# Optimization experiments

Hardware: AMD Instinct MI355X
Metric: run time of the kernel (lower is better)

The kernel has to match this reference:

```python
import jax, jax.numpy as jnp
import numpy as np

WS = 7          # window size
NH = 12         # num heads
DIM = 384       # channels
B, H, W = 16, 56, 56
N = WS * WS     # 49 tokens per window
HD = DIM // NH  # head dim = 32
SCALE = HD ** (-0.5)


def _rel_pos_index():
    # matches the numpy construction in Window_MSA.__init__
    coords = np.stack(np.meshgrid(np.arange(WS), np.arange(WS), indexing='ij'))
    flat = coords.reshape(2, -1)                      # [2, 49]
    rel = flat[:, :, None] - flat[:, None, :]         # [2, 49, 49]
    rel = rel.transpose(1, 2, 0)                      # [49, 49, 2]
    rel[:, :, 0] += WS - 1
    rel[:, :, 1] += WS - 1
    rel[:, :, 0] *= 2 * WS - 1
    return rel.sum(-1)                                # [49, 49] int

_REL_IDX = jnp.asarray(_rel_pos_index())


def setup_inputs() -> dict:
    key = jax.random.key(0)
    ks = jax.random.split(key, 4)
    return {
        'x': jax.random.normal(ks[0], (B, H, W, DIM), dtype=jnp.float32),
        'qkv_w': jax.random.normal(ks[1], (DIM, 3 * DIM), dtype=jnp.float32) * 0.02,
        'qkv_b': jnp.zeros((3 * DIM,), dtype=jnp.float32),
        'proj_w': jax.random.normal(ks[2], (DIM, DIM), dtype=jnp.float32) * 0.02,
        'proj_b': jnp.zeros((DIM,), dtype=jnp.float32),
        'rel_table': jax.random.normal(ks[3], ((2 * WS - 1) ** 2, NH), dtype=jnp.float32) * 0.02,
    }


def reference(x, qkv_w, qkv_b, proj_w, proj_b, rel_table):
    b, h, w, c = x.shape
    nwh, nww = h // WS, w // WS
    # window partition -> [B*nW, N, C]
    xw = x.reshape(b, nwh, WS, nww, WS, c).transpose(0, 1, 3, 2, 4, 5)
    xw = xw.reshape(-1, N, c)
    bn = xw.shape[0]
    # qkv projection -> q,k,v each [bn, NH, N, HD]
    qkv = (xw @ qkv_w + qkv_b).reshape(bn, N, 3, NH, HD).transpose(2, 0, 3, 1, 4)
    q, k, v = qkv[0] * SCALE, qkv[1], qkv[2]
    attn = jax.nn.softmax(jnp.einsum('bhnd,bhmd->bhnm', q, k), axis=-1)
    # NOTE: source adds relative position bias AFTER softmax (faithful quirk)
    bias = rel_table[_REL_IDX.reshape(-1)].reshape(N, N, NH).transpose(2, 0, 1)
    attn = attn + bias[None]
    out = jnp.einsum('bhnm,bhmd->bhnd', attn, v)
    out = out.transpose(0, 2, 1, 3).reshape(bn, N, c)
    out = out @ proj_w + proj_b
    # window reverse -> [B, H, W, C]
    out = out.reshape(b, nwh, nww, WS, WS, c).transpose(0, 1, 3, 2, 4, 5)
    return out.reshape(b, h, w, c)
```

## Files before the change

### kernel.cpp

```cpp
#include <hip/hip_runtime.h>
#include <hip/hip_bf16.h>

typedef unsigned short u16;
typedef __attribute__((ext_vector_type(8))) short bf16x8;
typedef __attribute__((ext_vector_type(4))) float f32x4;

#define NH 12
#define SCALE 0.1767766952966369f

#define UNIT 20992
#define WS_R0    ((size_t)0)
#define WS_QKVB  ((size_t)12288 * UNIT)
#define WS_PROJB (WS_QKVB + (size_t)3 * 12 * 49152)
#define WS_NEED  (WS_PROJB + (size_t)12 * 49152)

__device__ __forceinline__ void split2(float x, u16& h, u16& l) {
    __hip_bfloat16 hb = __float2bfloat16(x);
    float hf = __bfloat162float(hb);
    __hip_bfloat16 lb = __float2bfloat16(x - hf);
    h = __bfloat16_as_ushort(hb);
    l = __bfloat16_as_ushort(lb);
}
__device__ __forceinline__ void split8(const float* v, bf16x8& hi, bf16x8& lo) {
    #pragma unroll
    for (int j = 0; j < 8; ++j) {
        u16 h, l; split2(v[j], h, l);
        hi[j] = (short)h; lo[j] = (short)l;
    }
}

__device__ __forceinline__ void gload16(const char* g, char* l) {
    __builtin_amdgcn_global_load_lds(
        (const __attribute__((address_space(1))) unsigned*)g,
        (__attribute__((address_space(3))) unsigned*)l, 16, 0, 0);
}

__device__ __forceinline__ int swz(int row, int g) {
    return row * 128 + (((g ^ (row & 7)) & 7) << 4);
}

__global__ __launch_bounds__(384) void prep_kernel(
    const float* __restrict__ qkv_w, const float* __restrict__ proj_w,
    char* __restrict__ ws)
{
    const int b = blockIdx.x, row = threadIdx.x;
    float w; size_t base;
    int kl;
    if (b < 1152) {
        int s = b / 384, r = b % 384, ck = r / 32; kl = r % 32;
        w = qkv_w[(size_t)(ck * 32 + kl) * 1152 + s * 384 + row];
        base = WS_QKVB + (size_t)(s * 12 + ck) * 49152;
    } else {
        int b1 = b - 1152, ck = b1 / 32; kl = b1 % 32;
        w = proj_w[(size_t)(ck * 32 + kl) * 384 + row];
        base = WS_PROJB + (size_t)ck * 49152;
    }
    u16 h, l; split2(w, h, l);
    int o = ((row >> 4) * 4 + (kl >> 3)) * 256 + (row & 15) * 16 + (kl & 7) * 2;
    *(u16*)(ws + base + o)         = h;
    *(u16*)(ws + base + 24576 + o) = l;
}

__global__ __launch_bounds__(512, 4) void qkv_gemm_kernel(
    const float* __restrict__ x, const char* __restrict__ wsB,
    const float* __restrict__ qkv_b, char* __restrict__ ws)
{
    __shared__ __align__(16) char bt[49152];

    const int bid = blockIdx.x;
    const int nt = bid % 6, s = nt >> 1, lt = nt & 1;
    const int pair = bid / 6;
    const int tid = threadIdx.x, lane = tid & 63;
    const int wv = tid >> 6;
    const int wm = wv >> 1, wn = wv & 1;
    const int ln = lane & 15, kq = lane >> 4;

    const float* xr[2];
    #pragma unroll
    for (int am = 0; am < 2; ++am) {
        int wwin = pair * 2 + am;
        int bi = wwin >> 6, win = wwin & 63;
        int wy = win >> 3, wx = win & 7;
        int arow = wm * 16 + ln;
        int ar = (arow < 49) ? arow : 0;
        int Y = wy * 7 + ar / 7, X = wx * 7 + ar % 7;
        xr[am] = x + (size_t)((bi * 56 + Y) * 56 + X) * 384 + kq * 8;
    }
    const char* wB = wsB + WS_QKVB + (size_t)s * 12 * 49152;

    auto stage = [&](int ck, int buf) {
        const char* cb = wB + (size_t)ck * 49152 + (size_t)lt * 12288;
        #pragma unroll
        for (int i = 0; i < 3; ++i) {
            int seg = wv + i * 8;
            const char* src = (seg < 12) ? (cb + seg * 1024)
                                         : (cb + 24576 + (seg - 12) * 1024);
            gload16(src + lane * 16, bt + buf * 24576 + seg * 1024);
        }
    };

    stage(0, 0);
    float4 a0A = *(const float4*)(xr[0]);
    float4 a1A = *(const float4*)(xr[0] + 4);
    float4 a0B = *(const float4*)(xr[1]);
    float4 a1B = *(const float4*)(xr[1] + 4);
    __syncthreads();

    f32x4 acc[2][6];
    #pragma unroll
    for (int am = 0; am < 2; ++am)
        #pragma unroll
        for (int f = 0; f < 6; ++f) { acc[am][f][0]=0.f; acc[am][f][1]=0.f; acc[am][f][2]=0.f; acc[am][f][3]=0.f; }

    #pragma unroll 1
    for (int ck = 0; ck < 12; ++ck) {
        const int cur = (ck & 1) * 24576;
        float4 n0A, n1A, n0B, n1B;
        if (ck < 11) {
            stage(ck + 1, (ck & 1) ^ 1);
            n0A = *(const float4*)(xr[0] + (ck + 1) * 32);
            n1A = *(const float4*)(xr[0] + (ck + 1) * 32 + 4);
            n0B = *(const float4*)(xr[1] + (ck + 1) * 32);
            n1B = *(const float4*)(xr[1] + (ck + 1) * 32 + 4);
        }
        bf16x8 ah0, al0, ah1, al1;
        {
            float av[8];
            av[0]=a0A.x; av[1]=a0A.y; av[2]=a0A.z; av[3]=a0A.w;
            av[4]=a1A.x; av[5]=a1A.y; av[6]=a1A.z; av[7]=a1A.w;
            split8(av, ah0, al0);
            av[0]=a0B.x; av[1]=a0B.y; av[2]=a0B.z; av[3]=a0B.w;
            av[4]=a1B.x; av[5]=a1B.y; av[6]=a1B.z; av[7]=a1B.w;
            split8(av, ah1, al1);
        }
        #pragma unroll
        for (int f = 0; f < 6; ++f) {
            int off = cur + ((wn * 6 + f) * 4 + kq) * 256 + ln * 16;
            bf16x8 bh = *(const bf16x8*)(bt + off);
            bf16x8 bl = *(const bf16x8*)(bt + off + 12288);
            acc[0][f] = __builtin_amdgcn_mfma_f32_16x16x32_bf16(ah0, bh, acc[0][f], 0, 0, 0);
            acc[0][f] = __builtin_amdgcn_mfma_f32_16x16x32_bf16(ah0, bl, acc[0][f], 0, 0, 0);
            acc[0][f] = __builtin_amdgcn_mfma_f32_16x16x32_bf16(al0, bh, acc[0][f], 0, 0, 0);
            acc[1][f] = __builtin_amdgcn_mfma_f32_16x16x32_bf16(ah1, bh, acc[1][f], 0, 0, 0);
            acc[1][f] = __builtin_amdgcn_mfma_f32_16x16x32_bf16(ah1, bl, acc[1][f], 0, 0, 0);
            acc[1][f] = __builtin_amdgcn_mfma_f32_16x16x32_bf16(al1, bh, acc[1][f], 0, 0, 0);
        }
        __syncthreads();
        if (ck < 11) { a0A = n0A; a1A = n1A; a0B = n0B; a1B = n1B; }
    }

    #pragma unroll
    for (int am = 0; am < 2; ++am) {
        int wwin = pair * 2 + am;
        u16* ub = (u16*)(ws + WS_R0 + (size_t)(wwin * 12) * UNIT);
        #pragma unroll
        for (int f = 0; f < 6; ++f) {
            int n_local = lt * 192 + wn * 96 + f * 16 + ln;
            int hh = n_local >> 5, dd = n_local & 31;
            float bias = qkv_b[s * 384 + n_local];
            u16* u = ub + (size_t)hh * (UNIT / 2);
            #pragma unroll
            for (int r = 0; r < 4; ++r) {
                int wrow = wm * 16 + kq * 4 + r;
                if (wrow < 49) {
                    float val = acc[am][f][r] + bias;
                    if (s == 0) val *= SCALE;
                    u16 h, l; split2(val, h, l);
                    if (s == 0)      { u[wrow * 32 + dd] = h;        u[1568 + wrow * 32 + dd] = l; }
                    else if (s == 1) { u[3136 + wrow * 32 + dd] = h; u[4704 + wrow * 32 + dd] = l; }
                    else             { u[6272 + wrow * 32 + dd] = h; u[8320 + wrow * 32 + dd] = l; }
                }
            }
        }
    }
}

__global__ __launch_bounds__(256) void attn_core_kernel(
    const char* __restrict__ ws, const float* __restrict__ rel_table,
    float* __restrict__ out)
{
    __shared__ __align__(16) float pt[64][68];
    __shared__ __align__(16) float rel_all[2048];
    __shared__ float pmax[4][64];
    __shared__ float psum[4][64];
    __shared__ __align__(16) u16 vth[32][72];
    __shared__ __align__(16) u16 vtl[32][72];

    const int wi = blockIdx.x, bi = wi >> 6, win = wi & 63;
    const int wy = win >> 3, wx = win & 7;
    const int tid = threadIdx.x, lane = tid & 63, wv = tid >> 6;
    const int ln = lane & 15, kq = lane >> 4;

    for (int i = tid; i < 2028; i += 256) rel_all[i] = rel_table[i];
    for (int i = tid; i < 32 * 72; i += 256) { ((u16*)vth)[i] = 0; ((u16*)vtl)[i] = 0; }

    int m7[4], mr[4], outY[4], outX[4];
    bool mok[4];
    #pragma unroll
    for (int r = 0; r < 4; ++r) {
        int m = wv * 16 + kq * 4 + r;
        mok[r] = (m < 49);
        int a = mok[r] ? m : 0;
        m7[r] = a / 7; mr[r] = a % 7;
        outY[r] = wy * 7 + m7[r]; outX[r] = wx * 7 + mr[r];
    }
    int n7[4], nr[4];
    #pragma unroll
    for (int nt = 0; nt < 4; ++nt) {
        int n = nt * 16 + ln, a = (n < 49) ? n : 0;
        n7[nt] = a / 7; nr[nt] = a % 7;
    }
    const int mK = wv * 16 + ln;
    bf16x8 zz;
    #pragma unroll
    for (int j = 0; j < 8; ++j) zz[j] = 0;

    __syncthreads();

    for (int h = 0; h < NH; ++h) {
        const u16* u = (const u16*)(ws + WS_R0 + (size_t)(wi * 12 + h) * UNIT);
        const u16* qhi = u,        * qlo = u + 1568;
        const u16* khi = u + 3136, * klo = u + 4704;
        const u16* vhi = u + 6272, * vlo = u + 8320;

        if (tid < 196) {
            int row = tid >> 2, d0 = (tid & 3) * 8;
            bf16x8 v8h = *(const bf16x8*)(vhi + row * 32 + d0);
            bf16x8 v8l = *(const bf16x8*)(vlo + row * 32 + d0);
            #pragma unroll
            for (int j = 0; j < 8; ++j) {
                vth[d0 + j][row] = (u16)v8h[j];
                vtl[d0 + j][row] = (u16)v8l[j];
            }
        }

        bf16x8 kh = zz, kl = zz;
        if (mK < 49) {
            kh = *(const bf16x8*)(khi + mK * 32 + kq * 8);
            kl = *(const bf16x8*)(klo + mK * 32 + kq * 8);
        }
        f32x4 accs[4];
        #pragma unroll
        for (int nt = 0; nt < 4; ++nt) {
            int n = nt * 16 + ln;
            bf16x8 qh = zz, ql = zz;
            if (n < 49) {
                qh = *(const bf16x8*)(qhi + n * 32 + kq * 8);
                ql = *(const bf16x8*)(qlo + n * 32 + kq * 8);
            }
            f32x4 z; z[0]=0.f; z[1]=0.f; z[2]=0.f; z[3]=0.f;
            z = __builtin_amdgcn_mfma_f32_16x16x32_bf16(kh, qh, z, 0, 0, 0);
            z = __builtin_amdgcn_mfma_f32_16x16x32_bf16(kh, ql, z, 0, 0, 0);
            z = __builtin_amdgcn_mfma_f32_16x16x32_bf16(kl, qh, z, 0, 0, 0);
            accs[nt] = z;
        }

        float e[4][4], gmax[4], ginv[4];
        #pragma unroll
        for (int nt = 0; nt < 4; ++nt) {
            float lm = -3.4e38f;
            #pragma unroll
            for (int r = 0; r < 4; ++r) if (mok[r]) lm = fmaxf(lm, accs[nt][r]);
            lm = fmaxf(lm, __shfl_xor(lm, 16));
            lm = fmaxf(lm, __shfl_xor(lm, 32));
            if (kq == 0) pmax[wv][nt * 16 + ln] = lm;
        }
        __syncthreads();
        #pragma unroll
        for (int nt = 0; nt < 4; ++nt) {
            int n = nt * 16 + ln;
            gmax[nt] = fmaxf(fmaxf(pmax[0][n], pmax[1][n]), fmaxf(pmax[2][n], pmax[3][n]));
            float ls = 0.f;
            #pragma unroll
            for (int r = 0; r < 4; ++r) {
                e[nt][r] = mok[r] ? __expf(accs[nt][r] - gmax[nt]) : 0.f;
                ls += e[nt][r];
            }
            ls += __shfl_xor(ls, 16);
            ls += __shfl_xor(ls, 32);
            if (kq == 0) psum[wv][nt * 16 + ln] = ls;
        }
        __syncthreads();
        #pragma unroll
        for (int nt = 0; nt < 4; ++nt) {
            int n = nt * 16 + ln;
            ginv[nt] = 1.f / (psum[0][n] + psum[1][n] + psum[2][n] + psum[3][n]);
            #pragma unroll
            for (int r = 0; r < 4; ++r) {
                float val = 0.f;
                if (mok[r]) {
                    int bidx = (n7[nt] - m7[r] + 6) * 13 + (nr[nt] - mr[r] + 6);
                    val = e[nt][r] * ginv[nt] + rel_all[bidx * NH + h];
                }
                pt[n][wv * 16 + kq * 4 + r] = val;
            }
        }
        __syncthreads();

        bf16x8 pah[2], pal[2];
        #pragma unroll
        for (int mc = 0; mc < 2; ++mc) {
            const float* pp = &pt[wv * 16 + ln][mc * 32 + kq * 8];
            float v[8];
            float4 a0 = *(const float4*)pp;
            float4 a1 = *(const float4*)(pp + 4);
            v[0]=a0.x; v[1]=a0.y; v[2]=a0.z; v[3]=a0.w;
            v[4]=a1.x; v[5]=a1.y; v[6]=a1.z; v[7]=a1.w;
            split8(v, pah[mc], pal[mc]);
        }
        f32x4 acco[2];
        #pragma unroll
        for (int dt = 0; dt < 2; ++dt) { acco[dt][0]=0.f; acco[dt][1]=0.f; acco[dt][2]=0.f; acco[dt][3]=0.f; }
        #pragma unroll
        for (int dt = 0; dt < 2; ++dt) {
            int d = dt * 16 + ln;
            #pragma unroll
            for (int mc = 0; mc < 2; ++mc) {
                bf16x8 vh = *(const bf16x8*)(&vth[d][mc * 32 + kq * 8]);
                bf16x8 vl = *(const bf16x8*)(&vtl[d][mc * 32 + kq * 8]);
                acco[dt] = __builtin_amdgcn_mfma_f32_16x16x32_bf16(pah[mc], vh, acco[dt], 0, 0, 0);
                acco[dt] = __builtin_amdgcn_mfma_f32_16x16x32_bf16(pah[mc], vl, acco[dt], 0, 0, 0);
                acco[dt] = __builtin_amdgcn_mfma_f32_16x16x32_bf16(pal[mc], vh, acco[dt], 0, 0, 0);
            }
        }
        #pragma unroll
        for (int r = 0; r < 4; ++r) {
            if (mok[r]) {
                size_t base = (size_t)((bi * 56 + outY[r]) * 56 + outX[r]) * 384 + h * 32;
                out[base + ln]      = acco[0][r];
                out[base + 16 + ln] = acco[1][r];
            }
        }
        __syncthreads();
    }
}

__global__ __launch_bounds__(512) void proj_kernel(
    const char* __restrict__ wsB, const float* __restrict__ proj_b,
    float* __restrict__ out)
{
    __shared__ __align__(16) char bt[49152];

    const int tid = threadIdx.x, lane = tid & 63;
    const int wv = tid >> 6, wm = wv >> 1, wn = wv & 1;
    const int ln = lane & 15, kq = lane >> 4;
    const size_t tok0 = (size_t)blockIdx.x * 64;
    const float* xr = out + (tok0 + wm * 16 + ln) * 384 + kq * 8;
    const char* wB = wsB + WS_PROJB;

    bf16x8 st[6];
    #pragma unroll
    for (int i = 0; i < 6; ++i)
        st[i] = *(const bf16x8*)(wB + (size_t)tid * 16 + i * 8192);

    float4 a0 = *(const float4*)(xr);
    float4 a1 = *(const float4*)(xr + 4);

    f32x4 acc[12];
    #pragma unroll
    for (int f = 0; f < 12; ++f) { acc[f][0]=0.f; acc[f][1]=0.f; acc[f][2]=0.f; acc[f][3]=0.f; }

    #pragma unroll 1
    for (int ck = 0; ck < 12; ++ck) {
        __syncthreads();
        #pragma unroll
        for (int i = 0; i < 6; ++i)
            *(bf16x8*)(bt + tid * 16 + i * 8192) = st[i];
        __syncthreads();
        float4 na0, na1;
        if (ck < 11) {
            const char* nb = wB + (size_t)(ck + 1) * 49152;
            #pragma unroll
            for (int i = 0; i < 6; ++i)
                st[i] = *(const bf16x8*)(nb + (size_t)tid * 16 + i * 8192);
            na0 = *(const float4*)(xr + (ck + 1) * 32);
            na1 = *(const float4*)(xr + (ck + 1) * 32 + 4);
        }
        float av[8];
        av[0]=a0.x; av[1]=a0.y; av[2]=a0.z; av[3]=a0.w;
        av[4]=a1.x; av[5]=a1.y; av[6]=a1.z; av[7]=a1.w;
        bf16x8 ah, al; split8(av, ah, al);
        #pragma unroll
        for (int f = 0; f < 12; ++f) {
            int off = (wn * 12 + f) * 1024 + kq * 256 + ln * 16;
            bf16x8 bh = *(const bf16x8*)(bt + off);
            bf16x8 bl = *(const bf16x8*)(bt + 24576 + off);
            acc[f] = __builtin_amdgcn_mfma_f32_16x16x32_bf16(ah, bh, acc[f], 0, 0, 0);
            acc[f] = __builtin_amdgcn_mfma_f32_16x16x32_bf16(ah, bl, acc[f], 0, 0, 0);
            acc[f] = __builtin_amdgcn_mfma_f32_16x16x32_bf16(al, bh, acc[f], 0, 0, 0);
        }
        if (ck < 11) { a0 = na0; a1 = na1; }
    }
    __syncthreads();

    #pragma unroll
    for (int f = 0; f < 12; ++f) {
        int n = wn * 192 + f * 16 + ln;
        float pb = proj_b[n];
        #pragma unroll
        for (int r = 0; r < 4; ++r)
            out[(tok0 + wm * 16 + kq * 4 + r) * 384 + n] = acc[f][r] + pb;
    }
}

__global__ __launch_bounds__(512) void wmsa_attn_kernel(
    const float* __restrict__ x, const float* __restrict__ qkv_w,
    const float* __restrict__ qkv_b, const float* __restrict__ rel_table,
    float* __restrict__ out)
{
    __shared__ __align__(16) char smem[55936];
    u16* bt_hi = (u16*)smem;
    u16* bt_lo = (u16*)(smem + 24576);
    float* qs  = (float*)smem;
    float* kss = (float*)(smem + 14976);
    float* vst = (float*)(smem + 29952);
    float* at  = (float*)(smem + 44288);

    const int wi = blockIdx.x, bi = wi >> 6, win = wi & 63;
    const int wy = win >> 3, wx = win & 7;
    const int tid = threadIdx.x, lane = tid & 63;
    const int wv = tid >> 6, wm = wv >> 1, wn = wv & 1;
    const int ln = lane & 15, kq = lane >> 4;
    const int arow = wm * 16 + ln;

    int Y = wy * 7, X = wx * 7;
    if (arow < 49) { Y += arow / 7; X += arow % 7; }
    const float* xr = x + (size_t)((bi * 56 + Y) * 56 + X) * 384;

    int tcol[3], tkg[3];
    #pragma unroll
    for (int t = 0; t < 3; ++t) { int idx = tid + t * 512; tcol[t] = idx % 192; tkg[t] = idx / 192; }
    float rr[3][8];
    auto loadB = [&](int p, int ck) {
        #pragma unroll
        for (int t = 0; t < 3; ++t) {
            int c = tcol[t];
            int n = (c >> 6) * 384 + p * 64 + (c & 63);
            const float* wp = qkv_w + (size_t)(ck * 64 + tkg[t] * 8) * 1152 + n;
            #pragma unroll
            for (int j = 0; j < 8; ++j) rr[t][j] = wp[(size_t)j * 1152];
        }
    };
    loadB(0, 0);

    #pragma unroll 1
    for (int p = 0; p < 6; ++p) {
        f32x4 acc[6];
        #pragma unroll
        for (int f = 0; f < 6; ++f) { acc[f][0]=0.f; acc[f][1]=0.f; acc[f][2]=0.f; acc[f][3]=0.f; }
        #pragma unroll 1
        for (int ck = 0; ck < 6; ++ck) {
            __syncthreads();
            #pragma unroll
            for (int t = 0; t < 3; ++t) {
                bf16x8 h, l;
                split8(rr[t], h, l);
                *(bf16x8*)((char*)bt_hi + swz(tcol[t], tkg[t])) = h;
                *(bf16x8*)((char*)bt_lo + swz(tcol[t], tkg[t])) = l;
            }
            __syncthreads();
            if (ck < 5) loadB(p, ck + 1);
            else if (p < 5) loadB(p + 1, 0);
            #pragma unroll
            for (int ks = 0; ks < 2; ++ks) {
                float av[8];
                const float* xp = xr + ck * 64 + ks * 32 + kq * 8;
                float4 a0 = *(const float4*)xp;
                float4 a1 = *(const float4*)(xp + 4);
                av[0]=a0.x; av[1]=a0.y; av[2]=a0.z; av[3]=a0.w;
                av[4]=a1.x; av[5]=a1.y; av[6]=a1.z; av[7]=a1.w;
                bf16x8 ah, al; split8(av, ah, al);
                #pragma unroll
                for (int f = 0; f < 6; ++f) {
                    int n = wn * 96 + f * 16 + ln;
                    int off = swz(n, ks * 4 + kq);
                    bf16x8 bh = *(const bf16x8*)((char*)bt_hi + off);
                    bf16x8 bl = *(const bf16x8*)((char*)bt_lo + off);
                    acc[f] = __builtin_amdgcn_mfma_f32_16x16x32_bf16(ah, bh, acc[f], 0, 0, 0);
                    acc[f] = __builtin_amdgcn_mfma_f32_16x16x32_bf16(ah, bl, acc[f], 0, 0, 0);
                    acc[f] = __builtin_amdgcn_mfma_f32_16x16x32_bf16(al, bh, acc[f], 0, 0, 0);
                }
            }
        }
        __syncthreads();
        #pragma unroll
        for (int f = 0; f < 6; ++f) {
            int c = wn * 96 + f * 16 + ln;
            int m = c >> 6, d = c & 63, hh = d >> 5, dd = d & 31;
            float bias = qkv_b[m * 384 + p * 64 + d];
            #pragma unroll
            for (int r = 0; r < 4; ++r) {
                int row = wm * 16 + kq * 4 + r;
                if (row < 52) {
                    float val = acc[f][r] + bias;
                    if (m == 0)      qs [(hh * 52 + row) * 36 + dd] = val * SCALE;
                    else if (m == 1) kss[(hh * 52 + row) * 36 + dd] = val;
                    else             vst[(hh * 32 + dd) * 56 + row] = val;
                }
            }
        }
        __syncthreads();
        for (int hh = 0; hh < 2; ++hh) {
            const int h = p * 2 + hh;
            const float* qsh = qs  + hh * 52 * 36;
            const float* ksh = kss + hh * 52 * 36;
            const float* vsh = vst + hh * 32 * 56;
            if (tid < 169) {
                const int n0 = (tid / 13) * 4, m0 = (tid % 13) * 4;
                float s[4][4] = {};
                #pragma unroll
                for (int k = 0; k < 32; k += 4) {
                    float4 qa[4], kb[4];
                    #pragma unroll
                    for (int i = 0; i < 4; ++i) qa[i] = *(const float4*)&qsh[(n0 + i) * 36 + k];
                    #pragma unroll
                    for (int j = 0; j < 4; ++j) kb[j] = *(const float4*)&ksh[(m0 + j) * 36 + k];
                    #pragma unroll
                    for (int i = 0; i < 4; ++i)
                        #pragma unroll
                        for (int j = 0; j < 4; ++j)
                            s[i][j] += qa[i].x * kb[j].x + qa[i].y * kb[j].y +
                                       qa[i].z * kb[j].z + qa[i].w * kb[j].w;
                }
                #pragma unroll
                for (int i = 0; i < 4; ++i)
                    #pragma unroll
                    for (int j = 0; j < 4; ++j)
                        at[(n0 + i) * 56 + m0 + j] = s[i][j];
            }
            __syncthreads();
            for (int r = wv; r < 49; r += 8) {
                float v = (lane < 49) ? at[r * 56 + lane] : -3.4e38f;
                float mx = v;
                #pragma unroll
                for (int off = 32; off; off >>= 1) mx = fmaxf(mx, __shfl_xor(mx, off));
                float ex = (lane < 49) ? __expf(v - mx) : 0.f;
                float ssum = ex;
                #pragma unroll
                for (int off = 32; off; off >>= 1) ssum += __shfl_xor(ssum, off);
                if (lane < 52) {
                    float res = 0.f;
                    if (lane < 49) {
                        int py = r / 7, px = r % 7, qy = lane / 7, qx = lane % 7;
                        int bidx = (py - qy + 6) * 13 + (px - qx + 6);
                        res = ex / ssum + rel_table[bidx * NH + h];
                    }
                    at[r * 56 + lane] = res;
                }
            }
            __syncthreads();
            if (tid < 208) {
                const int n0 = (tid / 16) * 4, d0 = (tid % 16) * 2;
                float o[4][2] = {};
                #pragma unroll
                for (int m2 = 0; m2 < 52; m2 += 4) {
                    float4 pa[4], vb2[2];
                    #pragma unroll
                    for (int i = 0; i < 4; ++i) pa[i] = *(const float4*)&at[(n0 + i) * 56 + m2];
                    #pragma unroll
                    for (int j = 0; j < 2; ++j) vb2[j] = *(const float4*)&vsh[(d0 + j) * 56 + m2];
                    #pragma unroll
                    for (int i = 0; i < 4; ++i)
                        #pragma unroll
                        for (int j = 0; j < 2; ++j)
                            o[i][j] += pa[i].x * vb2[j].x + pa[i].y * vb2[j].y +
                                       pa[i].z * vb2[j].z + pa[i].w * vb2[j].w;
                }
                #pragma unroll
                for (int i = 0; i < 4; ++i) {
                    int n = n0 + i;
                    if (n < 49) {
                        int Yo = wy * 7 + n / 7, Xo = wx * 7 + n % 7;
                        size_t base = (size_t)((bi * 56 + Yo) * 56 + Xo) * 384 + h * 32 + d0;
                        *(float2*)(out + base) = make_float2(o[i][0], o[i][1]);
                    }
                }
            }
            __syncthreads();
        }
    }
}

__global__ __launch_bounds__(512) void wmsa_proj_kernel(
    const float* __restrict__ proj_w, const float* __restrict__ proj_b,
    float* __restrict__ out)
{
    __shared__ __align__(16) char smem[98304];
    u16* bt_hi = (u16*)smem;
    u16* bt_lo = (u16*)(smem + 49152);

    const int tid = threadIdx.x, lane = tid & 63;
    const int wv = tid >> 6, wm = wv >> 1, wn = wv & 1;
    const int ln = lane & 15, kq = lane >> 4;
    const size_t tok0 = (size_t)blockIdx.x * 64;
    const float* xr = out + (tok0 + wm * 16 + ln) * 384;

    int tcol[6], tkg[6];
    #pragma unroll
    for (int t = 0; t < 6; ++t) { int idx = tid + t * 512; tcol[t] = idx % 384; tkg[t] = idx / 384; }
    float rr[6][8];
    auto loadB = [&](int ck) {
        #pragma unroll
        for (int t = 0; t < 6; ++t) {
            const float* wp = proj_w + (size_t)(ck * 64 + tkg[t] * 8) * 384 + tcol[t];
            #pragma unroll
            for (int j = 0; j < 8; ++j) rr[t][j] = wp[(size_t)j * 384];
        }
    };
    loadB(0);

    f32x4 acc[12];
    #pragma unroll
    for (int f = 0; f < 12; ++f) { acc[f][0]=0.f; acc[f][1]=0.f; acc[f][2]=0.f; acc[f][3]=0.f; }

    #pragma unroll 1
    for (int ck = 0; ck < 6; ++ck) {
        __syncthreads();
        #pragma unroll
        for (int t = 0; t < 6; ++t) {
            bf16x8 h, l; split8(rr[t], h, l);
            *(bf16x8*)((char*)bt_hi + swz(tcol[t], tkg[t])) = h;
            *(bf16x8*)((char*)bt_lo + swz(tcol[t], tkg[t])) = l;
        }
        __syncthreads();
        if (ck < 5) loadB(ck + 1);
        #pragma unroll
        for (int ks = 0; ks < 2; ++ks) {
            float av[8];
            const float* xp = xr + ck * 64 + ks * 32 + kq * 8;
            float4 a0 = *(const float4*)xp;
            float4 a1 = *(const float4*)(xp + 4);
            av[0]=a0.x; av[1]=a0.y; av[2]=a0.z; av[3]=a0.w;
            av[4]=a1.x; av[5]=a1.y; av[6]=a1.z; av[7]=a1.w;
            bf16x8 ah, al; split8(av, ah, al);
            #pragma unroll
            for (int f = 0; f < 12; ++f) {
                int n = wn * 192 + f * 16 + ln;
                int off = swz(n, ks * 4 + kq);
                bf16x8 bh = *(const bf16x8*)((char*)bt_hi + off);
                bf16x8 bl = *(const bf16x8*)((char*)bt_lo + off);
                acc[f] = __builtin_amdgcn_mfma_f32_16x16x32_bf16(ah, bh, acc[f], 0, 0, 0);
                acc[f] = __builtin_amdgcn_mfma_f32_16x16x32_bf16(ah, bl, acc[f], 0, 0, 0);
                acc[f] = __builtin_amdgcn_mfma_f32_16x16x32_bf16(al, bh, acc[f], 0, 0, 0);
            }
        }
    }
    __syncthreads();

    #pragma unroll
    for (int f = 0; f < 12; ++f) {
        int n = wn * 192 + f * 16 + ln;
        float pb = proj_b[n];
        #pragma unroll
        for (int r = 0; r < 4; ++r)
            out[(tok0 + wm * 16 + kq * 4 + r) * 384 + n] = acc[f][r] + pb;
    }
}

extern "C" void kernel_launch(void* const* d_in, const int* in_sizes, int n_in,
                              void* d_out, int out_size, void* d_ws, size_t ws_size,
                              hipStream_t stream) {
    const float* x         = (const float*)d_in[0];
    const float* qkv_w     = (const float*)d_in[1];
    const float* qkv_b     = (const float*)d_in[2];
    const float* proj_w    = (const float*)d_in[3];
    const float* proj_b    = (const float*)d_in[4];
    const float* rel_table = (const float*)d_in[5];
    float* out = (float*)d_out;
    char* wsc = (char*)d_ws;

    if (ws_size >= WS_NEED) {
        hipLaunchKernelGGL(prep_kernel, dim3(1536), dim3(384), 0, stream,
                           qkv_w, proj_w, wsc);
        hipLaunchKernelGGL(qkv_gemm_kernel, dim3(3072), dim3(512), 0, stream,
                           x, wsc, qkv_b, wsc);
        hipLaunchKernelGGL(attn_core_kernel, dim3(1024), dim3(256), 0, stream,
                           wsc, rel_table, out);
        hipLaunchKernelGGL(proj_kernel, dim3(784), dim3(512), 0, stream,
                           wsc, proj_b, out);
    } else {
        hipLaunchKernelGGL(wmsa_attn_kernel, dim3(1024), dim3(512), 0, stream,
                           x, qkv_w, qkv_b, rel_table, out);
        hipLaunchKernelGGL(wmsa_proj_kernel, dim3(784), dim3(512), 0, stream,
                           proj_w, proj_b, out);
    }
}
```

Baseline: 438.8 us.

## Halve QKV GEMM N-tile and drop activation register prefetch for occupancy

Narrows each QKV GEMM block's output-column tile from 192 to 96 columns, doubling the grid and halving the shared-memory B buffer and accumulator count. It also removes the software prefetch of the next activation chunk into registers and loads x directly each iteration. The aim is more resident blocks per CU (launch bounds raised to 6) to hide latency. In exchange, each x tile is reloaded and re-split to bf16 by twice as many blocks, and x loads are no longer overlapped with compute.

```diff
diff --git a/kernel.cpp b/kernel.cpp
--- a/kernel.cpp
+++ b/kernel.cpp
@@ -61,15 +61,15 @@
     *(u16*)(ws + base + 24576 + o) = l;
 }
 
-__global__ __launch_bounds__(512, 4) void qkv_gemm_kernel(
+__global__ __launch_bounds__(512, 6) void qkv_gemm_kernel(
     const float* __restrict__ x, const char* __restrict__ wsB,
     const float* __restrict__ qkv_b, char* __restrict__ ws)
 {
-    __shared__ __align__(16) char bt[49152];
+    __shared__ __align__(16) char bt[24576];
 
     const int bid = blockIdx.x;
-    const int nt = bid % 6, s = nt >> 1, lt = nt & 1;
-    const int pair = bid / 6;
+    const int nt = bid % 12, s = nt >> 2, qt = nt & 3;
+    const int pair = bid / 12;
     const int tid = threadIdx.x, lane = tid & 63;
     const int wv = tid >> 6;
     const int wm = wv >> 1, wn = wv & 1;
@@ -89,55 +89,50 @@
     const char* wB = wsB + WS_QKVB + (size_t)s * 12 * 49152;
 
     auto stage = [&](int ck, int buf) {
-        const char* cb = wB + (size_t)ck * 49152 + (size_t)lt * 12288;
-        #pragma unroll
-        for (int i = 0; i < 3; ++i) {
+        const char* cb = wB + (size_t)ck * 49152 + (size_t)qt * 6144;
+        #pragma unroll
+        for (int i = 0; i < 2; ++i) {
             int seg = wv + i * 8;
-            const char* src = (seg < 12) ? (cb + seg * 1024)
-                                         : (cb + 24576 + (seg - 12) * 1024);
-            gload16(src + lane * 16, bt + buf * 24576 + seg * 1024);
+            if (seg < 12) {
+                const char* src = (seg < 6) ? (cb + seg * 1024)
+                                            : (cb + 24576 + (seg - 6) * 1024);
+                gload16(src + lane * 16, bt + buf * 12288 + seg * 1024);
+            }
         }
     };
 
     stage(0, 0);
-    float4 a0A = *(const float4*)(xr[0]);
-    float4 a1A = *(const float4*)(xr[0] + 4);
-    float4 a0B = *(const float4*)(xr[1]);
-    float4 a1B = *(const float4*)(xr[1] + 4);
     __syncthreads();
 
-    f32x4 acc[2][6];
+    f32x4 acc[2][3];
     #pragma unroll
     for (int am = 0; am < 2; ++am)
         #pragma unroll
-        for (int f = 0; f < 6; ++f) { acc[am][f][0]=0.f; acc[am][f][1]=0.f; acc[am][f][2]=0.f; acc[am][f][3]=0.f; }
+        for (int f = 0; f < 3; ++f) { acc[am][f][0]=0.f; acc[am][f][1]=0.f; acc[am][f][2]=0.f; acc[am][f][3]=0.f; }
 
     #pragma unroll 1
     for (int ck = 0; ck < 12; ++ck) {
-        const int cur = (ck & 1) * 24576;
-        float4 n0A, n1A, n0B, n1B;
-        if (ck < 11) {
-            stage(ck + 1, (ck & 1) ^ 1);
-            n0A = *(const float4*)(xr[0] + (ck + 1) * 32);
-            n1A = *(const float4*)(xr[0] + (ck + 1) * 32 + 4);
-            n0B = *(const float4*)(xr[1] + (ck + 1) * 32);
-            n1B = *(const float4*)(xr[1] + (ck + 1) * 32 + 4);
-        }
+        const int cur = (ck & 1) * 12288;
+        if (ck < 11) stage(ck + 1, (ck & 1) ^ 1);
         bf16x8 ah0, al0, ah1, al1;
         {
             float av[8];
-            av[0]=a0A.x; av[1]=a0A.y; av[2]=a0A.z; av[3]=a0A.w;
-            av[4]=a1A.x; av[5]=a1A.y; av[6]=a1A.z; av[7]=a1A.w;
+            float4 a0 = *(const float4*)(xr[0] + ck * 32);
+            float4 a1 = *(const float4*)(xr[0] + ck * 32 + 4);
+            av[0]=a0.x; av[1]=a0.y; av[2]=a0.z; av[3]=a0.w;
+            av[4]=a1.x; av[5]=a1.y; av[6]=a1.z; av[7]=a1.w;
             split8(av, ah0, al0);
-            av[0]=a0B.x; av[1]=a0B.y; av[2]=a0B.z; av[3]=a0B.w;
-            av[4]=a1B.x; av[5]=a1B.y; av[6]=a1B.z; av[7]=a1B.w;
+            a0 = *(const float4*)(xr[1] + ck * 32);
+            a1 = *(const float4*)(xr[1] + ck * 32 + 4);
+            av[0]=a0.x; av[1]=a0.y; av[2]=a0.z; av[3]=a0.w;
+            av[4]=a1.x; av[5]=a1.y; av[6]=a1.z; av[7]=a1.w;
             split8(av, ah1, al1);
         }
         #pragma unroll
-        for (int f = 0; f < 6; ++f) {
-            int off = cur + ((wn * 6 + f) * 4 + kq) * 256 + ln * 16;
+        for (int f = 0; f < 3; ++f) {
+            int off = cur + ((wn * 3 + f) * 4 + kq) * 256 + ln * 16;
             bf16x8 bh = *(const bf16x8*)(bt + off);
-            bf16x8 bl = *(const bf16x8*)(bt + off + 12288);
+            bf16x8 bl = *(const bf16x8*)(bt + off + 6144);
             acc[0][f] = __builtin_amdgcn_mfma_f32_16x16x32_bf16(ah0, bh, acc[0][f], 0, 0, 0);
             acc[0][f] = __builtin_amdgcn_mfma_f32_16x16x32_bf16(ah0, bl, acc[0][f], 0, 0, 0);
             acc[0][f] = __builtin_amdgcn_mfma_f32_16x16x32_bf16(al0, bh, acc[0][f], 0, 0, 0);
@@ -146,7 +141,6 @@
             acc[1][f] = __builtin_amdgcn_mfma_f32_16x16x32_bf16(al1, bh, acc[1][f], 0, 0, 0);
         }
         __syncthreads();
-        if (ck < 11) { a0A = n0A; a1A = n1A; a0B = n0B; a1B = n1B; }
     }
 
     #pragma unroll
@@ -154,8 +148,8 @@
         int wwin = pair * 2 + am;
         u16* ub = (u16*)(ws + WS_R0 + (size_t)(wwin * 12) * UNIT);
         #pragma unroll
-        for (int f = 0; f < 6; ++f) {
-            int n_local = lt * 192 + wn * 96 + f * 16 + ln;
+        for (int f = 0; f < 3; ++f) {
+            int n_local = qt * 96 + wn * 48 + f * 16 + ln;
             int hh = n_local >> 5, dd = n_local & 31;
             float bias = qkv_b[s * 384 + n_local];
             u16* u = ub + (size_t)hh * (UNIT / 2);
@@ -672,7 +666,7 @@
     if (ws_size >= WS_NEED) {
         hipLaunchKernelGGL(prep_kernel, dim3(1536), dim3(384), 0, stream,
                            qkv_w, proj_w, wsc);
-        hipLaunchKernelGGL(qkv_gemm_kernel, dim3(3072), dim3(512), 0, stream,
+        hipLaunchKernelGGL(qkv_gemm_kernel, dim3(6144), dim3(512), 0, stream,
                            x, wsc, qkv_b, wsc);
         hipLaunchKernelGGL(attn_core_kernel, dim3(1024), dim3(256), 0, stream,
                            wsc, rel_table, out);
```

Result: slower. 481.4 us (+9.7%).
